# Performance work log

Measured on AMD Instinct MI355X. Metric: run time of the kernel, lower is better.

The kernel has to match this reference:

```python
import jax, jax.numpy as jnp
import numpy as np

DIM = 1024
TOPK = 64
PAIRS = DIM // 2  # phase_pairs default
PHASE_MIX = 0.5
GATE_THRESHOLD = 0.0
EPS = 1e-12  # F.normalize default eps


def _l2norm(v):
    # matches F.normalize(v, dim=-1): v / max(||v||, eps)
    n = jnp.linalg.norm(v, axis=-1, keepdims=True)
    return v / jnp.maximum(n, EPS)


def setup_inputs() -> dict:
    key = jax.random.key(0)
    ks = jax.random.split(key, 6)
    s = 0.02  # small init scale for weights
    return {
        "x": jax.random.normal(ks[0], (4, 4096, DIM), dtype=jnp.float32),
        "gate_W": jax.random.normal(ks[1], (DIM, DIM), dtype=jnp.float32) * s,
        "gate_b": jnp.zeros((DIM,), dtype=jnp.float32),
        "mag_W": jax.random.normal(ks[2], (DIM, DIM), dtype=jnp.float32) * s,
        "mag_b": jnp.zeros((DIM,), dtype=jnp.float32),
        "Wq": jax.random.normal(ks[3], (DIM, DIM), dtype=jnp.float32) * s,
        "Wk": jax.random.normal(ks[4], (DIM, DIM), dtype=jnp.float32) * s,
        "phase_W": jax.random.normal(ks[5], (2 * PAIRS, DIM), dtype=jnp.float32) * s,
    }


def reference(x, gate_W, gate_b, mag_W, mag_b, Wq, Wk, phase_W):
    B, S, D = x.shape
    # gated SAE-style projection (gated=True, diag=False)
    gate_pre = x @ gate_W.T + gate_b          # [B,S,D]
    mag_pre = x @ mag_W.T + mag_b             # [B,S,D]
    # hard gate with straight-through estimator
    gate_soft = jax.nn.sigmoid(gate_pre)
    gate_hard = (gate_pre > GATE_THRESHOLD).astype(x.dtype)
    gate = gate_hard + gate_soft - jax.lax.stop_gradient(gate_soft)
    mag = jax.nn.relu(mag_pre)
    # top-k scatter mask along feature dim
    idx = jax.lax.top_k(gate_pre, TOPK)[1]    # [B,S,K]
    rows = jnp.arange(B * S)[:, None]
    mask = (jnp.zeros((B * S, D), dtype=bool)
            .at[rows, idx.reshape(B * S, TOPK)].set(True)
            .reshape(B, S, D))
    gate = jnp.where(mask, gate, jnp.zeros_like(gate))
    mag = jnp.where(mask, mag, jnp.zeros_like(mag))
    xg = gate * mag
    # twist projections, L2-normalized
    q = _l2norm(xg @ Wq.T)
    k = _l2norm(xg @ Wk.T)
    # symplectic momentum map over consecutive steps
    momentum_map = q[:, 1:] * k[:, :-1] - q[:, :-1] * k[:, 1:]  # [B,S-1,D]
    twist_mag = jnp.linalg.norm(momentum_map, axis=-1, keepdims=True)
    complexity = jnp.pad(jnp.tanh(twist_mag), ((0, 0), (1, 0), (0, 0)))  # [B,S,1]
    # phase branch (phase_mix > 0)
    phase = (xg @ phase_W.T).reshape(B, S, PAIRS, 2)
    phase = _l2norm(phase)
    pp, pc = phase[:, :-1], phase[:, 1:]
    cross = pp[..., 0] * pc[..., 1] - pp[..., 1] * pc[..., 0]   # [B,S-1,P]
    dot = jnp.clip(jnp.sum(pp * pc, axis=-1), -1.0, 1.0)
    phase_delta = jnp.abs(jnp.arctan2(cross, dot)) / jnp.pi
    phase_score = jnp.pad(jnp.mean(phase_delta, axis=-1, keepdims=True),
                          ((0, 0), (1, 0), (0, 0)))             # [B,S,1]
    return (1.0 - PHASE_MIX) * complexity + PHASE_MIX * phase_score
```

## Files before the change

### kernel.cpp

```cpp
#include <hip/hip_runtime.h>
#include <math.h>

#define DIM 1024
#define ROWS 16384
#define SEQ 4096
#define MARGIN 0.012f
#define MAXC 24

typedef __bf16 v8bf __attribute__((ext_vector_type(8)));
typedef float v4f __attribute__((ext_vector_type(4)));
typedef int v8i __attribute__((ext_vector_type(8)));

__device__ __forceinline__ unsigned short f2bf(float f){
  unsigned u = __float_as_uint(f);
  u = u + 0x7FFFu + ((u >> 16) & 1u);
  return (unsigned short)(u >> 16);
}
__device__ __forceinline__ float bf2f(unsigned short h){
  return __uint_as_float(((unsigned)h) << 16);
}
__device__ __forceinline__ unsigned short relu_bf(unsigned short h){
  return (h & 0x8000u) ? (unsigned short)0 : h;
}
__device__ __forceinline__ unsigned f2fp8(float f){
  float a = fabsf(f);
  unsigned sign = (__float_as_uint(f) >> 24) & 0x80u;
  if (a >= 448.f) return sign | 0x7Eu;
  if (a < 0.015625f){
    int k = (int)rintf(a * 512.f);
    if (k >= 8) return sign | 0x08u;
    return sign | (unsigned)k;
  }
  unsigned u = __float_as_uint(a);
  u += 0x7FFFFu + ((u >> 20) & 1u);
  int e = (int)((u >> 23) & 0xFFu) - 127;
  unsigned m = (u >> 20) & 7u;
  if (e > 8) return sign | 0x7Eu;
  return sign | ((unsigned)(e + 7) << 3) | m;
}
__device__ __forceinline__ void lds_fence(){
  __asm__ volatile("s_waitcnt lgkmcnt(0)" ::: "memory");
}

__global__ __launch_bounds__(256) void cvt_all(
    const float* __restrict__ x,
    const float* __restrict__ w0, const float* __restrict__ w1,
    const float* __restrict__ w2, const float* __restrict__ w3,
    const float* __restrict__ w4,
    unsigned short* __restrict__ xbf, unsigned short* __restrict__ wbf,
    unsigned char* __restrict__ wf8){
  const int y = blockIdx.y;
  int i = (blockIdx.x * 256 + threadIdx.x) * 4;
  if (y < 16){
    const float* s = x + ((size_t)y << 20);
    float4 f = *(const float4*)(s + i);
    ushort4 o; o.x = f2bf(f.x); o.y = f2bf(f.y); o.z = f2bf(f.z); o.w = f2bf(f.w);
    *(ushort4*)(xbf + ((size_t)y << 20) + i) = o;
  } else if (y < 18){
    const float* s = (y == 16) ? w0 : w1;
    float4 f = *(const float4*)(s + i);
    ushort4 o; o.x = f2bf(f.x); o.y = f2bf(f.y); o.z = f2bf(f.z); o.w = f2bf(f.w);
    *(ushort4*)(wbf + ((size_t)(y - 16) << 20) + i) = o;
  } else {
    const float* s = (y == 18) ? w2 : ((y == 19) ? w3 : w4);
    float4 f = *(const float4*)(s + i);
    unsigned u = f2fp8(f.x * 32.f) | (f2fp8(f.y * 32.f) << 8) |
                 (f2fp8(f.z * 32.f) << 16) | (f2fp8(f.w * 32.f) << 24);
    *(unsigned*)(wf8 + ((size_t)(y - 18) << 20) + i) = u;
  }
}

__global__ __launch_bounds__(256, 4) void gemm_bt(
    const unsigned short* __restrict__ A, const unsigned short* __restrict__ B,
    const float* __restrict__ bias0, const float* __restrict__ bias1,
    void* __restrict__ C0, void* __restrict__ C1, void* __restrict__ C2,
    int bf16mask)
{
  __shared__ unsigned short lA[128 * 32];
  __shared__ unsigned short lB[128 * 32];
  const int t = threadIdx.x;
  const int lane = t & 63, wave = t >> 6;
  const int bid = blockIdx.y * gridDim.x + blockIdx.x;
  const int m0 = (bid & 127) * 128;
  const int n0 = (bid >> 7) * 128;
  const int wm = (wave >> 1) * 64, wn = (wave & 1) * 64;
  const int ar = lane & 15, aq = lane >> 4;

  v4f acc[4][4];
#pragma unroll
  for (int i = 0; i < 4; i++)
#pragma unroll
    for (int j = 0; j < 4; j++) acc[i][j] = v4f{0.f, 0.f, 0.f, 0.f};

  for (int k0 = 0; k0 < DIM; k0 += 32){
#pragma unroll
    for (int i = 0; i < 2; i++){
      int c = (wave * 2 + i) * 64 + lane;
      int row = c >> 2, kq = c & 3;
      __builtin_amdgcn_global_load_lds(
        (const __attribute__((address_space(1))) void*)(A + (size_t)(m0 + row) * DIM + k0 + kq * 8),
        (__attribute__((address_space(3))) void*)(&lA[c * 8]), 16, 0, 0);
      __builtin_amdgcn_global_load_lds(
        (const __attribute__((address_space(1))) void*)(B + (size_t)(n0 + row) * DIM + k0 + kq * 8),
        (__attribute__((address_space(3))) void*)(&lB[c * 8]), 16, 0, 0);
    }
    __syncthreads();
    v8bf af[4], bf[4];
#pragma unroll
    for (int i = 0; i < 4; i++){
      af[i] = *(const v8bf*)&lA[(wm + i * 16 + ar) * 32 + aq * 8];
      bf[i] = *(const v8bf*)&lB[(wn + i * 16 + ar) * 32 + aq * 8];
    }
#pragma unroll
    for (int mi = 0; mi < 4; mi++)
#pragma unroll
      for (int ni = 0; ni < 4; ni++)
        acc[mi][ni] = __builtin_amdgcn_mfma_f32_16x16x32_bf16(af[mi], bf[ni], acc[mi][ni], 0, 0, 0);
    __syncthreads();
  }

  const int os = n0 >> 10;
  void* Cp = (os == 0) ? C0 : ((os == 1) ? C1 : C2);
  const float* bp = (os == 0) ? bias0 : ((os == 1) ? bias1 : nullptr);
  const bool half_out = ((bf16mask >> os) & 1) != 0;
#pragma unroll
  for (int mi = 0; mi < 4; mi++)
#pragma unroll
    for (int ni = 0; ni < 4; ni++){
      int col = (n0 + wn + ni * 16 + ar) & (DIM - 1);
      float bv = bp ? bp[col] : 0.f;
#pragma unroll
      for (int rr = 0; rr < 4; rr++){
        int rowg = m0 + wm + mi * 16 + aq * 4 + rr;
        float val = acc[mi][ni][rr] + bv;
        if (half_out) ((unsigned short*)Cp)[(size_t)rowg * DIM + col] = f2bf(val);
        else          ((float*)Cp)[(size_t)rowg * DIM + col] = val;
      }
    }
}

__global__ __launch_bounds__(256, 3) void gemm8(
    const unsigned char* __restrict__ A, const unsigned char* __restrict__ B,
    unsigned short* __restrict__ C0, unsigned short* __restrict__ C1,
    unsigned short* __restrict__ C2)
{
  __shared__ unsigned char lA[128 * 128];
  __shared__ unsigned char lB[128 * 128];
  const int t = threadIdx.x;
  const int lane = t & 63, wave = t >> 6;
  const int bid = blockIdx.y * gridDim.x + blockIdx.x;
  const int m0 = (bid & 127) * 128;
  const int n0 = (bid >> 7) * 128;
  const int wm = (wave >> 1) * 64, wn = (wave & 1) * 64;
  const int ar = lane & 15, aq = lane >> 4;

  v4f acc[4][4];
#pragma unroll
  for (int i = 0; i < 4; i++)
#pragma unroll
    for (int j = 0; j < 4; j++) acc[i][j] = v4f{0.f, 0.f, 0.f, 0.f};

  for (int k0 = 0; k0 < DIM; k0 += 128){
#pragma unroll
    for (int i = 0; i < 4; i++){
      int c = (wave * 4 + i) * 64 + lane;
      int row = c >> 3, kq = c & 7;
      __builtin_amdgcn_global_load_lds(
        (const __attribute__((address_space(1))) void*)(A + (size_t)(m0 + row) * DIM + k0 + kq * 16),
        (__attribute__((address_space(3))) void*)(&lA[c * 16]), 16, 0, 0);
      __builtin_amdgcn_global_load_lds(
        (const __attribute__((address_space(1))) void*)(B + (size_t)(n0 + row) * DIM + k0 + kq * 16),
        (__attribute__((address_space(3))) void*)(&lB[c * 16]), 16, 0, 0);
    }
    __syncthreads();
    v8i a8[4], b8[4];
#pragma unroll
    for (int i = 0; i < 4; i++){
      a8[i] = *(const v8i*)&lA[(wm + i * 16 + ar) * 128 + aq * 32];
      b8[i] = *(const v8i*)&lB[(wn + i * 16 + ar) * 128 + aq * 32];
    }
#pragma unroll
    for (int mi = 0; mi < 4; mi++)
#pragma unroll
      for (int ni = 0; ni < 4; ni++)
        acc[mi][ni] = __builtin_amdgcn_mfma_scale_f32_16x16x128_f8f6f4(
            a8[mi], b8[ni], acc[mi][ni], 0, 0, 0, 127u, 0, 127u);
    __syncthreads();
  }

  const int os = n0 >> 10;
  unsigned short* Cp = (os == 0) ? C0 : ((os == 1) ? C1 : C2);
#pragma unroll
  for (int mi = 0; mi < 4; mi++)
#pragma unroll
    for (int ni = 0; ni < 4; ni++){
      int col = (n0 + wn + ni * 16 + ar) & (DIM - 1);
#pragma unroll
      for (int rr = 0; rr < 4; rr++){
        int rowg = m0 + wm + mi * 16 + aq * 4 + rr;
        Cp[(size_t)rowg * DIM + col] = f2bf(acc[mi][ni][rr] * 0.03125f);
      }
    }
}

__global__ __launch_bounds__(256) void select_k(
  const unsigned short* __restrict__ gate_pre, const unsigned short* __restrict__ mag_pre,
  const float* __restrict__ x, const float* __restrict__ gW, const float* __restrict__ gb,
  unsigned char* __restrict__ xg8)
{
  __shared__ int   s_cnt[4];
  __shared__ int   s_idx[4][MAXC];
  __shared__ float s_ex [4][MAXC];
  __shared__ int   s_res[4][MAXC];

  const int t = threadIdx.x;
  const int lane = t & 63, wave = t >> 6;
  const int r = blockIdx.x * 4 + wave;
  const size_t rb = (size_t)r * DIM;

  float vg[16], vx[16];
  unsigned short mg[16];
#pragma unroll
  for (int c = 0; c < 4; c++){
    ushort4 g4 = *(const ushort4*)(gate_pre + rb + c * 256 + lane * 4);
    float4 x4 = *(const float4*)(x          + rb + c * 256 + lane * 4);
    ushort4 m4 = *(const ushort4*)(mag_pre  + rb + c * 256 + lane * 4);
    vg[c*4+0]=bf2f(g4.x); vg[c*4+1]=bf2f(g4.y); vg[c*4+2]=bf2f(g4.z); vg[c*4+3]=bf2f(g4.w);
    vx[c*4+0]=x4.x; vx[c*4+1]=x4.y; vx[c*4+2]=x4.z; vx[c*4+3]=x4.w;
    mg[c*4+0]=m4.x; mg[c*4+1]=m4.y; mg[c*4+2]=m4.z; mg[c*4+3]=m4.w;
  }
  if (lane == 0) s_cnt[wave] = 0;

  float lo = -8.f, hi = 8.f;
#pragma unroll
  for (int it = 0; it < 15; it++){
    float mid = 0.5f * (lo + hi);
    int cn = 0;
#pragma unroll
    for (int e = 0; e < 16; e++) cn += (vg[e] > mid) ? 1 : 0;
#pragma unroll
    for (int m = 32; m; m >>= 1) cn += __shfl_xor(cn, m);
    if (cn >= 64) lo = mid; else hi = mid;
  }
  const float cl = lo - MARGIN, ch = hi + MARGIN;

  int n1 = 0;
#pragma unroll
  for (int e = 0; e < 16; e++) n1 += (vg[e] > ch) ? 1 : 0;
#pragma unroll
  for (int m = 32; m; m >>= 1) n1 += __shfl_xor(n1, m);
  const int s = 64 - n1;

  lds_fence();
#pragma unroll
  for (int e = 0; e < 16; e++){
    float vv = vg[e];
    if (vv >= cl && vv <= ch){
      int p = atomicAdd(&s_cnt[wave], 1);
      if (p < MAXC) s_idx[wave][p] = (e >> 2) * 256 + lane * 4 + (e & 3);
    }
  }
  lds_fence();
  int namb = s_cnt[wave]; if (namb > MAXC) namb = MAXC;

  for (int i = 0; i < namb; i++){
    int d = s_idx[wave][i];
    const float* wr = gW + (size_t)d * DIM;
    float p = 0.f;
#pragma unroll
    for (int c = 0; c < 4; c++){
      float4 w4 = *(const float4*)(wr + c * 256 + lane * 4);
      p = fmaf(vx[c*4+0], w4.x, p); p = fmaf(vx[c*4+1], w4.y, p);
      p = fmaf(vx[c*4+2], w4.z, p); p = fmaf(vx[c*4+3], w4.w, p);
    }
#pragma unroll
    for (int m = 32; m; m >>= 1) p += __shfl_xor(p, m);
    if (lane == 0) s_ex[wave][i] = p + gb[d];
  }
  lds_fence();

  if (lane < namb){
    float e = s_ex[wave][lane]; int d = s_idx[wave][lane];
    int rank = 0;
    for (int j = 0; j < namb; j++){
      float ej = s_ex[wave][j]; int dj = s_idx[wave][j];
      if (ej > e || (ej == e && dj < d)) rank++;
    }
    s_res[wave][lane] = (rank < s && e > 0.f) ? 1 : 0;
  }
  lds_fence();

  float vals[16];
#pragma unroll
  for (int e = 0; e < 16; e++)
    vals[e] = (vg[e] > ch && vg[e] > 0.f) ? bf2f(relu_bf(mg[e])) : 0.f;
  for (int i = 0; i < namb; i++){
    int d = s_idx[wave][i];
    int res = s_res[wave][i];
    if (((d >> 2) & 63) == lane){
      int e = (d >> 8) * 4 + (d & 3);
      vals[e] = res ? bf2f(relu_bf(mg[e])) : 0.f;
    }
  }
#pragma unroll
  for (int c = 0; c < 4; c++){
    unsigned u = f2fp8(vals[c*4+0]) | (f2fp8(vals[c*4+1]) << 8) |
                 (f2fp8(vals[c*4+2]) << 16) | (f2fp8(vals[c*4+3]) << 24);
    *(unsigned*)(xg8 + rb + c * 256 + lane * 4) = u;
  }
}

__global__ __launch_bounds__(256) void epilogue_k(
  const unsigned short* __restrict__ q_pre, const unsigned short* __restrict__ k_pre,
  const unsigned short* __restrict__ p_pre, float* __restrict__ out)
{
  const int r0 = blockIdx.x * 4;
  const int t = threadIdx.x;
  const int lane = t & 63, wave = t >> 6;
  __shared__ float red[16];

  const int rp = (r0 == 0) ? 0 : r0 - 1;
  float vqp[4], vkp[4], vpp[4];
  {
    ushort4 uq = *(const ushort4*)(q_pre + (size_t)rp * DIM + 4*t);
    ushort4 uk = *(const ushort4*)(k_pre + (size_t)rp * DIM + 4*t);
    ushort4 up = *(const ushort4*)(p_pre + (size_t)rp * DIM + 4*t);
    vqp[0]=bf2f(uq.x); vqp[1]=bf2f(uq.y); vqp[2]=bf2f(uq.z); vqp[3]=bf2f(uq.w);
    vkp[0]=bf2f(uk.x); vkp[1]=bf2f(uk.y); vkp[2]=bf2f(uk.z); vkp[3]=bf2f(uk.w);
    vpp[0]=bf2f(up.x); vpp[1]=bf2f(up.y); vpp[2]=bf2f(up.z); vpp[3]=bf2f(up.w);
  }
  float aq = 0.f, ak = 0.f;
#pragma unroll
  for (int j = 0; j < 4; j++){ aq = fmaf(vqp[j], vqp[j], aq); ak = fmaf(vkp[j], vkp[j], ak); }
#pragma unroll
  for (int m = 32; m; m >>= 1){ aq += __shfl_xor(aq, m); ak += __shfl_xor(ak, m); }
  if (lane == 0){ red[wave] = aq; red[4 + wave] = ak; }
  __syncthreads();
  float rqp = 1.f / fmaxf(sqrtf(red[0] + red[1] + red[2] + red[3]), 1e-12f);
  float rkp = 1.f / fmaxf(sqrtf(red[4] + red[5] + red[6] + red[7]), 1e-12f);
  __syncthreads();

  for (int rr = 0; rr < 4; rr++){
    const int r = r0 + rr;
    float vqc[4], vkc[4], vpc[4];
    {
      ushort4 uq = *(const ushort4*)(q_pre + (size_t)r * DIM + 4*t);
      ushort4 uk = *(const ushort4*)(k_pre + (size_t)r * DIM + 4*t);
      ushort4 up = *(const ushort4*)(p_pre + (size_t)r * DIM + 4*t);
      vqc[0]=bf2f(uq.x); vqc[1]=bf2f(uq.y); vqc[2]=bf2f(uq.z); vqc[3]=bf2f(uq.w);
      vkc[0]=bf2f(uk.x); vkc[1]=bf2f(uk.y); vkc[2]=bf2f(uk.z); vkc[3]=bf2f(uk.w);
      vpc[0]=bf2f(up.x); vpc[1]=bf2f(up.y); vpc[2]=bf2f(up.z); vpc[3]=bf2f(up.w);
    }
    const bool seg = (r & (SEQ - 1)) == 0;
    float aqc = 0.f, akc = 0.f;
#pragma unroll
    for (int j = 0; j < 4; j++){ aqc = fmaf(vqc[j], vqc[j], aqc); akc = fmaf(vkc[j], vkc[j], akc); }
    float dsum = 0.f;
    if (!seg){
#pragma unroll
      for (int j = 0; j < 2; j++){
        float ax = vpp[2*j], ay = vpp[2*j+1], bx = vpc[2*j], by = vpc[2*j+1];
        float ia = 1.f / fmaxf(sqrtf(ax * ax + ay * ay), 1e-12f);
        float ib = 1.f / fmaxf(sqrtf(bx * bx + by * by), 1e-12f);
        ax *= ia; ay *= ia; bx *= ib; by *= ib;
        float cross = ax * by - ay * bx;
        float dot = fminf(fmaxf(ax * bx + ay * by, -1.f), 1.f);
        dsum += fabsf(atan2f(cross, dot)) * 0.3183098861837907f;
      }
    }
#pragma unroll
    for (int m = 32; m; m >>= 1){
      aqc += __shfl_xor(aqc, m); akc += __shfl_xor(akc, m); dsum += __shfl_xor(dsum, m);
    }
    if (lane == 0){ red[wave] = aqc; red[4 + wave] = akc; red[8 + wave] = dsum; }
    __syncthreads();
    float rqc = 1.f / fmaxf(sqrtf(red[0] + red[1] + red[2] + red[3]), 1e-12f);
    float rkc = 1.f / fmaxf(sqrtf(red[4] + red[5] + red[6] + red[7]), 1e-12f);
    if (!seg){
      float tw = 0.f;
#pragma unroll
      for (int j = 0; j < 4; j++){
        float m = (vqc[j] * rqc) * (vkp[j] * rkp) - (vqp[j] * rqp) * (vkc[j] * rkc);
        tw = fmaf(m, m, tw);
      }
#pragma unroll
      for (int m = 32; m; m >>= 1) tw += __shfl_xor(tw, m);
      if (lane == 0) red[12 + wave] = tw;
      __syncthreads();
      if (t == 0){
        float dtot = red[8] + red[9] + red[10] + red[11];
        float twt = red[12] + red[13] + red[14] + red[15];
        out[r] = 0.5f * tanhf(sqrtf(twt)) + 0.5f * (dtot * (1.f / 512.f));
      }
    } else {
      if (t == 0) out[r] = 0.f;
    }
    __syncthreads();
#pragma unroll
    for (int j = 0; j < 4; j++){ vqp[j] = vqc[j]; vkp[j] = vkc[j]; vpp[j] = vpc[j]; }
    rqp = rqc; rkp = rkc;
  }
}

extern "C" void kernel_launch(void* const* d_in, const int* in_sizes, int n_in,
                              void* d_out, int out_size, void* d_ws, size_t ws_size,
                              hipStream_t stream)
{
  const float* x       = (const float*)d_in[0];
  const float* gate_W  = (const float*)d_in[1];
  const float* gate_b  = (const float*)d_in[2];
  const float* mag_W   = (const float*)d_in[3];
  const float* mag_b   = (const float*)d_in[4];
  const float* Wq      = (const float*)d_in[5];
  const float* Wk      = (const float*)d_in[6];
  const float* phase_W = (const float*)d_in[7];
  float* out = (float*)d_out;

  char* ws = (char*)d_ws;
  unsigned short* xbf = (unsigned short*)ws;
  unsigned short* wbf = (unsigned short*)(ws + 33554432);
  unsigned char*  wf8 = (unsigned char*)(ws + 37748736);
  unsigned short* gate_pre = (unsigned short*)(ws + 41943040);
  unsigned short* mag_pre  = (unsigned short*)(ws + 75497472);
  unsigned short* p_pre    = (unsigned short*)(ws + 109051904);
  unsigned short* q_pre = gate_pre;
  unsigned short* k_pre = mag_pre;

  dim3 b256(256);
  cvt_all<<<dim3(1024, 21), b256, 0, stream>>>(x, gate_W, mag_W, Wq, Wk, phase_W,
                                               xbf, wbf, wf8);

  gemm_bt<<<dim3(16, 128), b256, 0, stream>>>(xbf, wbf, gate_b, mag_b,
                                              gate_pre, mag_pre, nullptr, 0b011);

  unsigned char* xg8 = (unsigned char*)xbf;
  select_k<<<ROWS / 4, b256, 0, stream>>>(gate_pre, mag_pre, x, gate_W, gate_b, xg8);

  gemm8<<<dim3(24, 128), b256, 0, stream>>>(xg8, wf8, q_pre, k_pre, p_pre);

  epilogue_k<<<ROWS / 4, b256, 0, stream>>>(q_pre, k_pre, p_pre, out);
}
```

Before: 390.1 us.

## Rewrite bf16 gate/mag GEMM as 256x256 double-buffered pipelined kernel

Replaces the simple 128x128-tile bf16 GEMM, which synchronised twice per 32-wide k step, with a 512-thread 256x256-tile kernel. It uses 128KB of dynamic LDS with double buffering, XOR-swizzled LDS layout, interleaved global_load_lds prefetches between MFMA phases, s_setprio, and a block-index swizzle for L2 locality. The aim is to hide global load latency, cut LDS bank conflicts and barrier overhead, and raise MFMA utilisation for the first GEMM. In exchange it brings heavy register pressure from 32 accumulators, manual waitcnt correctness risk, and only 512 blocks per launch.

```diff
diff --git a/kernel.cpp b/kernel.cpp
--- a/kernel.cpp
+++ b/kernel.cpp
@@ -70,73 +70,153 @@
   }
 }
 
-__global__ __launch_bounds__(256, 4) void gemm_bt(
+#define GBAR() asm volatile("s_barrier" ::: "memory")
+#define GLGKM0() { asm volatile("s_waitcnt lgkmcnt(0)" ::: "memory"); __builtin_amdgcn_sched_barrier(0); }
+#define GVM4() asm volatile("s_waitcnt vmcnt(4)" ::: "memory")
+
+__global__ __launch_bounds__(512, 2) void gemm_bt(
     const unsigned short* __restrict__ A, const unsigned short* __restrict__ B,
     const float* __restrict__ bias0, const float* __restrict__ bias1,
-    void* __restrict__ C0, void* __restrict__ C1, void* __restrict__ C2,
-    int bf16mask)
+    unsigned short* __restrict__ C0, unsigned short* __restrict__ C1)
 {
-  __shared__ unsigned short lA[128 * 32];
-  __shared__ unsigned short lB[128 * 32];
+  extern __shared__ unsigned char lds[];
   const int t = threadIdx.x;
   const int lane = t & 63, wave = t >> 6;
-  const int bid = blockIdx.y * gridDim.x + blockIdx.x;
-  const int m0 = (bid & 127) * 128;
-  const int n0 = (bid >> 7) * 128;
-  const int wm = (wave >> 1) * 64, wn = (wave & 1) * 64;
+  const int wr = wave >> 2, wc = wave & 3;
+  const int bid = blockIdx.x;
+  const int swz = (bid & 7) * 64 + (bid >> 3);
+  const int m0 = (swz & 63) * 256;
+  const int n0 = (swz >> 6) * 256;
+
+  int offv[4];
+#pragma unroll
+  for (int h = 0; h < 2; h++)
+#pragma unroll
+    for (int i = 0; i < 2; i++){
+      int o = h * 16384 + i * 8192 + t * 16;
+      int u = o ^ (((o >> 9) & 1) << 5);
+      int r = ((u >> 11) << 4) | ((u >> 6) & 15);
+      int c = (((u >> 10) & 1) << 5) | ((u & 63) >> 1);
+      offv[h * 2 + i] = r * 1024 + c;
+    }
+  const int off00 = offv[0], off01 = offv[1], off10 = offv[2], off11 = offv[3];
+  const unsigned short* Ab = A + ((size_t)m0 << 10);
+  const unsigned short* Bb = B + ((size_t)n0 << 10);
+
+  const int laneterm = (lane & 15) * 64 + (((lane >> 4) * 16) ^ (((lane >> 3) & 1) * 32));
+  const int aBase = wr * 16384 + laneterm;
+  const int bBase = 32768 + wc * 8192 + laneterm;
+
+#define GLD1(srcp, dsto) __builtin_amdgcn_global_load_lds( \
+    (const __attribute__((address_space(1))) void*)(srcp), \
+    (__attribute__((address_space(3))) void*)(lds + (dsto)), 16, 0, 0)
+
+  auto stageA = [&](int h, int kt, int pp){
+    const int o0 = h ? off10 : off00, o1 = h ? off11 : off01;
+    GLD1(Ab + o0 + kt * 64, pp * 65536 + h * 16384 + t * 16);
+    GLD1(Ab + o1 + kt * 64, pp * 65536 + h * 16384 + 8192 + t * 16);
+  };
+  auto stageB = [&](int h, int kt, int pp){
+    const int o0 = h ? off10 : off00, o1 = h ? off11 : off01;
+    GLD1(Bb + o0 + kt * 64, pp * 65536 + 32768 + h * 16384 + t * 16);
+    GLD1(Bb + o1 + kt * 64, pp * 65536 + 32768 + h * 16384 + 8192 + t * 16);
+  };
+
+  v4f acc[8][4];
+#pragma unroll
+  for (int i = 0; i < 8; i++)
+#pragma unroll
+    for (int j = 0; j < 4; j++) acc[i][j] = v4f{0.f, 0.f, 0.f, 0.f};
+
+  stageB(0, 0, 0); stageB(1, 0, 0);
+  stageA(0, 0, 0); stageA(1, 0, 0);
+  stageB(0, 1, 1); stageB(1, 1, 1);
+  GVM4();
+  GBAR();
+
+  int p = 0;
+  for (int X = 0; X < 16; X++, p ^= 1){
+    const int pb = p * 65536;
+    const int ktA = (X + 1 < 16) ? X + 1 : 15;
+    const int ktB = (X + 2 < 16) ? X + 2 : X;
+    v8bf a0[8], a1[8], b0[4], b1[4];
+
+#pragma unroll
+    for (int mi = 0; mi < 8; mi++) a0[mi] = *(const v8bf*)(lds + pb + aBase + mi * 2048);
+#pragma unroll
+    for (int ni = 0; ni < 4; ni++) b0[ni] = *(const v8bf*)(lds + pb + bBase + ni * 2048);
+    stageA(0, ktA, p ^ 1);
+    GBAR();
+    __builtin_amdgcn_s_setprio(1);
+#pragma unroll
+    for (int mi = 0; mi < 4; mi++)
+#pragma unroll
+      for (int ni = 0; ni < 4; ni++)
+        acc[mi][ni] = __builtin_amdgcn_mfma_f32_16x16x32_bf16(a0[mi], b0[ni], acc[mi][ni], 0, 0, 0);
+    __builtin_amdgcn_s_setprio(0);
+    GBAR();
+
+#pragma unroll
+    for (int mi = 0; mi < 4; mi++) a1[mi] = *(const v8bf*)(lds + pb + aBase + 1024 + mi * 2048);
+#pragma unroll
+    for (int ni = 0; ni < 4; ni++) b1[ni] = *(const v8bf*)(lds + pb + bBase + 1024 + ni * 2048);
+    stageA(1, ktA, p ^ 1);
+    GBAR();
+    __builtin_amdgcn_s_setprio(1);
+#pragma unroll
+    for (int mi = 0; mi < 4; mi++)
+#pragma unroll
+      for (int ni = 0; ni < 4; ni++)
+        acc[4 + mi][ni] = __builtin_amdgcn_mfma_f32_16x16x32_bf16(a0[4 + mi], b0[ni], acc[4 + mi][ni], 0, 0, 0);
+    __builtin_amdgcn_s_setprio(0);
+    GLGKM0();
+    GBAR();
+
+#pragma unroll
+    for (int mi = 4; mi < 8; mi++) a1[mi] = *(const v8bf*)(lds + pb + aBase + 1024 + mi * 2048);
+    stageB(0, ktB, p);
+    GBAR();
+    __builtin_amdgcn_s_setprio(1);
+#pragma unroll
+    for (int mi = 0; mi < 4; mi++)
+#pragma unroll
+      for (int ni = 0; ni < 4; ni++)
+        acc[mi][ni] = __builtin_amdgcn_mfma_f32_16x16x32_bf16(a1[mi], b1[ni], acc[mi][ni], 0, 0, 0);
+    __builtin_amdgcn_s_setprio(0);
+    GBAR();
+
+    stageB(1, ktB, p);
+    GBAR();
+    __builtin_amdgcn_s_setprio(1);
+#pragma unroll
+    for (int mi = 0; mi < 4; mi++)
+#pragma unroll
+      for (int ni = 0; ni < 4; ni++)
+        acc[4 + mi][ni] = __builtin_amdgcn_mfma_f32_16x16x32_bf16(a1[4 + mi], b1[ni], acc[4 + mi][ni], 0, 0, 0);
+    __builtin_amdgcn_s_setprio(0);
+    GVM4();
+    GBAR();
+  }
+
+  const int os = n0 >> 10;
+  unsigned short* Cp = (os == 0) ? C0 : C1;
+  const float* bp = (os == 0) ? bias0 : bias1;
   const int ar = lane & 15, aq = lane >> 4;
-
-  v4f acc[4][4];
-#pragma unroll
-  for (int i = 0; i < 4; i++)
-#pragma unroll
-    for (int j = 0; j < 4; j++) acc[i][j] = v4f{0.f, 0.f, 0.f, 0.f};
-
-  for (int k0 = 0; k0 < DIM; k0 += 32){
-#pragma unroll
-    for (int i = 0; i < 2; i++){
-      int c = (wave * 2 + i) * 64 + lane;
-      int row = c >> 2, kq = c & 3;
-      __builtin_amdgcn_global_load_lds(
-        (const __attribute__((address_space(1))) void*)(A + (size_t)(m0 + row) * DIM + k0 + kq * 8),
-        (__attribute__((address_space(3))) void*)(&lA[c * 8]), 16, 0, 0);
-      __builtin_amdgcn_global_load_lds(
-        (const __attribute__((address_space(1))) void*)(B + (size_t)(n0 + row) * DIM + k0 + kq * 8),
-        (__attribute__((address_space(3))) void*)(&lB[c * 8]), 16, 0, 0);
-    }
-    __syncthreads();
-    v8bf af[4], bf[4];
-#pragma unroll
-    for (int i = 0; i < 4; i++){
-      af[i] = *(const v8bf*)&lA[(wm + i * 16 + ar) * 32 + aq * 8];
-      bf[i] = *(const v8bf*)&lB[(wn + i * 16 + ar) * 32 + aq * 8];
-    }
-#pragma unroll
-    for (int mi = 0; mi < 4; mi++)
-#pragma unroll
-      for (int ni = 0; ni < 4; ni++)
-        acc[mi][ni] = __builtin_amdgcn_mfma_f32_16x16x32_bf16(af[mi], bf[ni], acc[mi][ni], 0, 0, 0);
-    __syncthreads();
-  }
-
-  const int os = n0 >> 10;
-  void* Cp = (os == 0) ? C0 : ((os == 1) ? C1 : C2);
-  const float* bp = (os == 0) ? bias0 : ((os == 1) ? bias1 : nullptr);
-  const bool half_out = ((bf16mask >> os) & 1) != 0;
-#pragma unroll
-  for (int mi = 0; mi < 4; mi++)
-#pragma unroll
-    for (int ni = 0; ni < 4; ni++){
-      int col = (n0 + wn + ni * 16 + ar) & (DIM - 1);
-      float bv = bp ? bp[col] : 0.f;
+  const int ncol0 = (n0 & (DIM - 1)) + wc * 64;
+#pragma unroll
+  for (int ni = 0; ni < 4; ni++){
+    const int col = ncol0 + ni * 16 + ar;
+    const float bv = bp[col];
+#pragma unroll
+    for (int mi = 0; mi < 8; mi++){
 #pragma unroll
       for (int rr = 0; rr < 4; rr++){
-        int rowg = m0 + wm + mi * 16 + aq * 4 + rr;
-        float val = acc[mi][ni][rr] + bv;
-        if (half_out) ((unsigned short*)Cp)[(size_t)rowg * DIM + col] = f2bf(val);
-        else          ((float*)Cp)[(size_t)rowg * DIM + col] = val;
+        int rowg = m0 + wr * 128 + mi * 16 + aq * 4 + rr;
+        Cp[(size_t)rowg * DIM + col] = f2bf(acc[mi][ni][rr] + bv);
       }
     }
+  }
+  asm volatile("s_waitcnt vmcnt(0)" ::: "memory");
 }
 
 __global__ __launch_bounds__(256, 3) void gemm8(
@@ -426,12 +506,19 @@
   unsigned short* q_pre = gate_pre;
   unsigned short* k_pre = mag_pre;
 
+  static bool attr_set = false;
+  if (!attr_set){
+    hipFuncSetAttribute((const void*)gemm_bt,
+                        hipFuncAttributeMaxDynamicSharedMemorySize, 131072);
+    attr_set = true;
+  }
+
   dim3 b256(256);
   cvt_all<<<dim3(1024, 21), b256, 0, stream>>>(x, gate_W, mag_W, Wq, Wk, phase_W,
                                                xbf, wbf, wf8);
 
-  gemm_bt<<<dim3(16, 128), b256, 0, stream>>>(xbf, wbf, gate_b, mag_b,
-                                              gate_pre, mag_pre, nullptr, 0b011);
+  gemm_bt<<<dim3(512), dim3(512), 131072, stream>>>(xbf, wbf, gate_b, mag_b,
+                                                    gate_pre, mag_pre);
 
   unsigned char* xg8 = (unsigned char*)xbf;
   select_k<<<ROWS / 4, b256, 0, stream>>>(gate_pre, mag_pre, x, gate_W, gate_b, xg8);
```

Measured after the change: 385.3 us. About the same (-1.2%).
